# Performance work log

Hardware: AMD Instinct MI355X
Metric: run time of the kernel (lower is better)

The kernel has to match this reference:

```python
import jax, jax.numpy as jnp
import numpy as np


def setup_inputs() -> dict:
    key = jax.random.key(0)
    k1, k2, k3 = jax.random.split(key, 3)
    x = jax.random.normal(k1, (128, 3, 16, 64, 64), dtype=jnp.float32)
    conv_weight = jax.random.normal(k2, (24, 3, 3, 3, 3), dtype=jnp.float32) * 0.1
    conv_bias = jax.random.normal(k3, (24,), dtype=jnp.float32) * 0.1
    return {"x": x, "conv_weight": conv_weight, "conv_bias": conv_bias}


def reference(x, conv_weight, conv_bias):
    # Conv3d, stride=1, padding=0 (VALID), dilation=1, groups=1, NCDHW layout
    y = jax.lax.conv_general_dilated(
        x, conv_weight,
        window_strides=(1, 1, 1),
        padding='VALID',
        dimension_numbers=('NCDHW', 'OIDHW', 'NCDHW'),
    )
    y = y + conv_bias[None, :, None, None, None]  # [B, 24, 14, 62, 62]
    y = jnp.min(y, axis=2)                        # min over depth -> [B, 24, 62, 62]
    return jax.nn.softmax(y, axis=1)              # softmax over channels
```

## Files before the change

### kernel.cpp

```cpp
#include <hip/hip_runtime.h>
#include <math.h>

#define CIN   3
#define DIN   16
#define HWIN  64
#define COUT  24
#define DOUT  14
#define HOUT  62
#define WOUT  62

#define TILE_H  4
#define NTILES  16
#define NTHR    384
#define ROWS_IN 6
#define RP      68
#define PLANE_F (CIN * ROWS_IN * RP)
#define XSLAB_F (DIN * PLANE_F)
#define WOFF    XSLAB_F
#define WQ_F    324
#define LDS_F   (XSLAB_F + 6 * WQ_F)
#define SM_RP     64
#define SM_STRIDE (TILE_H * SM_RP)


__device__ __forceinline__ void gload_lds_dw(const float* g, float* l) {
    __builtin_amdgcn_global_load_lds(
        (const __attribute__((address_space(1))) unsigned int*)g,
        (__attribute__((address_space(3))) unsigned int*)l, 4, 0, 0);
}

__global__ __launch_bounds__(NTHR, 1) void conv_min_softmax_v6(
    const float* __restrict__ x,
    const float* __restrict__ w,
    const float* __restrict__ bias,
    float* __restrict__ out)
{
    __shared__ __align__(16) float smem[LDS_F];

    const int tid  = threadIdx.x;
    const int bid  = blockIdx.x;
    const int rt   = bid & (NTILES - 1);
    const int b    = bid >> 4;

    const int q    = __builtin_amdgcn_readfirstlane(tid >> 6);
    const int lane = tid & 63;
    const int r    = lane >> 4;
    const int wg   = lane & 15;
    const int q4   = q * 4;

    for (int i = tid; i < COUT * 81; i += NTHR) {
        const int co   = i / 81;
        const int rem  = i % 81;
        const int cin  = rem / 27;
        const int rem2 = rem % 27;
        const int kd   = rem2 / 9;
        const int kh   = (rem2 % 9) / 3;
        const int kw   = rem2 % 3;
        smem[WOFF + (co >> 2) * WQ_F + (cin * 3 + kh) * 36 + (kd * 3 + kw) * 4 + (co & 3)] = w[i];
    }
    const float bia0 = bias[q4 + 0], bia1 = bias[q4 + 1],
                bia2 = bias[q4 + 2], bia3 = bias[q4 + 3];

    const int grow = min(rt * TILE_H + q, HWIN - 1);
    const float* __restrict__ xrow =
        x + (size_t)b * (CIN * DIN * HWIN * HWIN) + grow * HWIN + lane;
    #pragma unroll
    for (int c = 0; c < CIN; ++c)
        #pragma unroll
        for (int p = 0; p < DIN; ++p)
            gload_lds_dw(xrow + (c * DIN + p) * (HWIN * HWIN),
                         &smem[p * PLANE_F + (c * ROWS_IN + q) * RP]);

    __syncthreads();

    float m[4][4];
    #pragma unroll
    for (int cop = 0; cop < 4; ++cop)
        #pragma unroll
        for (int i = 0; i < 4; ++i) m[cop][i] = 1e30f;

    const int vbase = r * RP + wg * 4;
    const float* __restrict__ wqb = &smem[WOFF + q * WQ_F];

    #pragma unroll 1
    for (int ch = 0; ch < 2; ++ch) {
        const int p0 = 7 * ch;

        float acc[7][4][4];
        #pragma unroll
        for (int d = 0; d < 7; ++d)
            #pragma unroll
            for (int cop = 0; cop < 4; ++cop)
                #pragma unroll
                for (int i = 0; i < 4; ++i) acc[d][cop][i] = 0.f;

        #pragma unroll 1
        for (int cin = 0; cin < CIN; ++cin) {
            #pragma unroll 1
            for (int kh = 0; kh < 3; ++kh) {
                const float* __restrict__ bp =
                    &smem[p0 * PLANE_F + cin * (ROWS_IN * RP) + kh * RP + vbase];
                const float* __restrict__ wp = wqb + (cin * 3 + kh) * 36;

                float wv[9][4];
                #pragma unroll
                for (int t = 0; t < 9; ++t)
                    *(float4*)wv[t] = *(const float4*)(wp + t * 4);

                #pragma unroll
                for (int pp = 0; pp < 9; ++pp) {
                    const float* rp2 = bp + pp * PLANE_F;
                    const float4 a4 = *(const float4*)rp2;
                    const float2 a2 = *(const float2*)(rp2 + 4);
                    const float xr[6] = { a4.x, a4.y, a4.z, a4.w, a2.x, a2.y };
                    #pragma unroll
                    for (int kd = 0; kd < 3; ++kd) {
                        if (pp - kd < 0 || pp - kd > 6) continue;
                        const int dzr = pp - kd;
                        #pragma unroll
                        for (int kw = 0; kw < 3; ++kw) {
                            #pragma unroll
                            for (int cop = 0; cop < 4; ++cop) {
                                const float wvv = wv[kd * 3 + kw][cop];
                                #pragma unroll
                                for (int i = 0; i < 4; ++i)
                                    acc[dzr][cop][i] = fmaf(wvv, xr[i + kw], acc[dzr][cop][i]);
                            }
                        }
                    }
                }
            }
        }

        #pragma unroll
        for (int d = 0; d < 7; ++d)
            #pragma unroll
            for (int cop = 0; cop < 4; ++cop)
                #pragma unroll
                for (int i = 0; i < 4; ++i)
                    m[cop][i] = fminf(m[cop][i], acc[d][cop][i]);
    }

    __syncthreads();

    {
        const int p = r * SM_RP + wg * 4;
        float4 v0 = { m[0][0] + bia0, m[0][1] + bia0, m[0][2] + bia0, m[0][3] + bia0 };
        float4 v1 = { m[1][0] + bia1, m[1][1] + bia1, m[1][2] + bia1, m[1][3] + bia1 };
        float4 v2 = { m[2][0] + bia2, m[2][1] + bia2, m[2][2] + bia2, m[2][3] + bia2 };
        float4 v3 = { m[3][0] + bia3, m[3][1] + bia3, m[3][2] + bia3, m[3][3] + bia3 };
        *(float4*)&smem[(q4 + 0) * SM_STRIDE + p] = v0;
        *(float4*)&smem[(q4 + 1) * SM_STRIDE + p] = v1;
        *(float4*)&smem[(q4 + 2) * SM_STRIDE + p] = v2;
        *(float4*)&smem[(q4 + 3) * SM_STRIDE + p] = v3;
    }
    __syncthreads();

    if (tid < 256) {
        const int row = tid >> 6;
        const int col = tid & 63;
        const int ho  = rt * TILE_H + row;
        if (col < WOUT && ho < HOUT) {
            float v[COUT];
            float mx = -1e30f;
            #pragma unroll
            for (int c = 0; c < COUT; ++c) {
                v[c] = smem[c * SM_STRIDE + row * SM_RP + col];
                mx = fmaxf(mx, v[c]);
            }
            float s = 0.f;
            #pragma unroll
            for (int c = 0; c < COUT; ++c) { v[c] = __expf(v[c] - mx); s += v[c]; }
            const float inv = 1.f / s;
            float* ob = out + (size_t)b * COUT * (HOUT * WOUT) + ho * WOUT + col;
            #pragma unroll
            for (int c = 0; c < COUT; ++c)
                ob[(size_t)c * (HOUT * WOUT)] = v[c] * inv;
        }
    }
}

extern "C" void kernel_launch(void* const* d_in, const int* in_sizes, int n_in,
                              void* d_out, int out_size, void* d_ws, size_t ws_size,
                              hipStream_t stream) {
    const float* x    = (const float*)d_in[0];
    const float* w    = (const float*)d_in[1];
    const float* bias = (const float*)d_in[2];
    float* out = (float*)d_out;

    conv_min_softmax_v6<<<128 * NTILES, NTHR, 0, stream>>>(x, w, bias, out);
}
```

Before: 498.3 us.

## Split output channels across eight waves, three per wave, with smaller depth chunks

Moves from 6 waves of 4 output channels each to 8 waves of 3 channels each (512 threads). The depth loop is split into chunks of 4,4,3,3 so the accumulator arrays shrink, and launch bounds request 2 blocks per CU. The input-slab load is redistributed across all 8 waves. The goal is more waves in flight per CU to hide LDS and FMA latency. The cost is that each weight float4 load now carries only 3 useful lanes, more halo input rows are reloaded across the smaller chunks, and LDS use per block may limit residency to one block.

Measured after the change: 476.8 us. 4.3% less time.

```diff
diff --git a/kernel.cpp b/kernel.cpp
--- a/kernel.cpp
+++ b/kernel.cpp
@@ -11,14 +11,14 @@
 
 #define TILE_H  4
 #define NTILES  16
-#define NTHR    384
+#define NTHR    512
 #define ROWS_IN 6
 #define RP      68
 #define PLANE_F (CIN * ROWS_IN * RP)
 #define XSLAB_F (DIN * PLANE_F)
 #define WOFF    XSLAB_F
-#define WQ_F    324
-#define LDS_F   (XSLAB_F + 6 * WQ_F)
+#define WT_F    324
+#define LDS_F   (XSLAB_F + 8 * WT_F)
 #define SM_RP     64
 #define SM_STRIDE (TILE_H * SM_RP)
 
@@ -29,7 +29,65 @@
         (__attribute__((address_space(3))) unsigned int*)l, 4, 0, 0);
 }
 
-__global__ __launch_bounds__(NTHR, 1) void conv_min_softmax_v6(
+template<int C>
+__device__ __forceinline__ void do_chunk(const float* __restrict__ xv,
+                                         const float* __restrict__ wqb,
+                                         float (&m)[3][4], const int p0)
+{
+    float acc[C][3][4];
+    #pragma unroll
+    for (int d = 0; d < C; ++d)
+        #pragma unroll
+        for (int cop = 0; cop < 3; ++cop)
+            #pragma unroll
+            for (int i = 0; i < 4; ++i) acc[d][cop][i] = 0.f;
+
+    #pragma unroll 1
+    for (int cin = 0; cin < CIN; ++cin) {
+        #pragma unroll 1
+        for (int kh = 0; kh < 3; ++kh) {
+            const float* __restrict__ bp = xv + p0 * PLANE_F + cin * (ROWS_IN * RP) + kh * RP;
+            const float* __restrict__ wp = wqb + (cin * 3 + kh) * 36;
+
+            float4 wv[9];
+            #pragma unroll
+            for (int t = 0; t < 9; ++t) wv[t] = *(const float4*)(wp + t * 4);
+
+            #pragma unroll
+            for (int pp = 0; pp < C + 2; ++pp) {
+                const float* rp2 = bp + pp * PLANE_F;
+                const float4 a4 = *(const float4*)rp2;
+                const float2 a2 = *(const float2*)(rp2 + 4);
+                const float xr[6] = { a4.x, a4.y, a4.z, a4.w, a2.x, a2.y };
+                #pragma unroll
+                for (int kd = 0; kd < 3; ++kd) {
+                    const int d = pp - kd;
+                    if (d < 0 || d >= C) continue;
+                    #pragma unroll
+                    for (int kw = 0; kw < 3; ++kw) {
+                        const float4 wt = wv[kd * 3 + kw];
+                        const float wc[3] = { wt.x, wt.y, wt.z };
+                        #pragma unroll
+                        for (int cop = 0; cop < 3; ++cop)
+                            #pragma unroll
+                            for (int i = 0; i < 4; ++i)
+                                acc[d][cop][i] = fmaf(wc[cop], xr[i + kw], acc[d][cop][i]);
+                    }
+                }
+            }
+        }
+    }
+
+    #pragma unroll
+    for (int d = 0; d < C; ++d)
+        #pragma unroll
+        for (int cop = 0; cop < 3; ++cop)
+            #pragma unroll
+            for (int i = 0; i < 4; ++i)
+                m[cop][i] = fminf(m[cop][i], acc[d][cop][i]);
+}
+
+__global__ __launch_bounds__(NTHR, 2) void conv_min_softmax_v7(
     const float* __restrict__ x,
     const float* __restrict__ w,
     const float* __restrict__ bias,
@@ -46,7 +104,7 @@
     const int lane = tid & 63;
     const int r    = lane >> 4;
     const int wg   = lane & 15;
-    const int q4   = q * 4;
+    const int q3   = q * 3;
 
     for (int i = tid; i < COUT * 81; i += NTHR) {
         const int co   = i / 81;
@@ -56,103 +114,50 @@
         const int kd   = rem2 / 9;
         const int kh   = (rem2 % 9) / 3;
         const int kw   = rem2 % 3;
-        smem[WOFF + (co >> 2) * WQ_F + (cin * 3 + kh) * 36 + (kd * 3 + kw) * 4 + (co & 3)] = w[i];
+        smem[WOFF + (co / 3) * WT_F + (cin * 3 + kh) * 36 + (kd * 3 + kw) * 4 + (co % 3)] = w[i];
     }
-    const float bia0 = bias[q4 + 0], bia1 = bias[q4 + 1],
-                bia2 = bias[q4 + 2], bia3 = bias[q4 + 3];
+    const float bia[3] = { bias[q3 + 0], bias[q3 + 1], bias[q3 + 2] };
 
-    const int grow = min(rt * TILE_H + q, HWIN - 1);
-    const float* __restrict__ xrow =
-        x + (size_t)b * (CIN * DIN * HWIN * HWIN) + grow * HWIN + lane;
-    #pragma unroll
-    for (int c = 0; c < CIN; ++c)
+    {
+        const float* __restrict__ xb =
+            x + (size_t)b * (CIN * DIN * HWIN * HWIN) + lane;
         #pragma unroll
-        for (int p = 0; p < DIN; ++p)
-            gload_lds_dw(xrow + (c * DIN + p) * (HWIN * HWIN),
-                         &smem[p * PLANE_F + (c * ROWS_IN + q) * RP]);
-
+        for (int k = 0; k < 36; ++k) {
+            const int p    = 2 * q + (k >= 18 ? 1 : 0);
+            const int sub  = k % 18;
+            const int cin  = sub / 6;
+            const int row  = sub % 6;
+            const int grow = min(rt * TILE_H + row, HWIN - 1);
+            gload_lds_dw(xb + ((cin * DIN + p) * (HWIN * HWIN) + grow * HWIN),
+                         &smem[p * PLANE_F + (cin * ROWS_IN + row) * RP]);
+        }
+    }
     __syncthreads();
 
-    float m[4][4];
+    float m[3][4];
     #pragma unroll
-    for (int cop = 0; cop < 4; ++cop)
+    for (int cop = 0; cop < 3; ++cop)
         #pragma unroll
         for (int i = 0; i < 4; ++i) m[cop][i] = 1e30f;
 
-    const int vbase = r * RP + wg * 4;
-    const float* __restrict__ wqb = &smem[WOFF + q * WQ_F];
+    const float* __restrict__ xv  = &smem[r * RP + wg * 4];
+    const float* __restrict__ wqb = &smem[WOFF + q * WT_F];
 
-    #pragma unroll 1
-    for (int ch = 0; ch < 2; ++ch) {
-        const int p0 = 7 * ch;
-
-        float acc[7][4][4];
-        #pragma unroll
-        for (int d = 0; d < 7; ++d)
-            #pragma unroll
-            for (int cop = 0; cop < 4; ++cop)
-                #pragma unroll
-                for (int i = 0; i < 4; ++i) acc[d][cop][i] = 0.f;
-
-        #pragma unroll 1
-        for (int cin = 0; cin < CIN; ++cin) {
-            #pragma unroll 1
-            for (int kh = 0; kh < 3; ++kh) {
-                const float* __restrict__ bp =
-                    &smem[p0 * PLANE_F + cin * (ROWS_IN * RP) + kh * RP + vbase];
-                const float* __restrict__ wp = wqb + (cin * 3 + kh) * 36;
-
-                float wv[9][4];
-                #pragma unroll
-                for (int t = 0; t < 9; ++t)
-                    *(float4*)wv[t] = *(const float4*)(wp + t * 4);
-
-                #pragma unroll
-                for (int pp = 0; pp < 9; ++pp) {
-                    const float* rp2 = bp + pp * PLANE_F;
-                    const float4 a4 = *(const float4*)rp2;
-                    const float2 a2 = *(const float2*)(rp2 + 4);
-                    const float xr[6] = { a4.x, a4.y, a4.z, a4.w, a2.x, a2.y };
-                    #pragma unroll
-                    for (int kd = 0; kd < 3; ++kd) {
-                        if (pp - kd < 0 || pp - kd > 6) continue;
-                        const int dzr = pp - kd;
-                        #pragma unroll
-                        for (int kw = 0; kw < 3; ++kw) {
-                            #pragma unroll
-                            for (int cop = 0; cop < 4; ++cop) {
-                                const float wvv = wv[kd * 3 + kw][cop];
-                                #pragma unroll
-                                for (int i = 0; i < 4; ++i)
-                                    acc[dzr][cop][i] = fmaf(wvv, xr[i + kw], acc[dzr][cop][i]);
-                            }
-                        }
-                    }
-                }
-            }
-        }
-
-        #pragma unroll
-        for (int d = 0; d < 7; ++d)
-            #pragma unroll
-            for (int cop = 0; cop < 4; ++cop)
-                #pragma unroll
-                for (int i = 0; i < 4; ++i)
-                    m[cop][i] = fminf(m[cop][i], acc[d][cop][i]);
-    }
+    do_chunk<4>(xv, wqb, m, 0);
+    do_chunk<4>(xv, wqb, m, 4);
+    do_chunk<3>(xv, wqb, m, 8);
+    do_chunk<3>(xv, wqb, m, 11);
 
     __syncthreads();
 
     {
         const int p = r * SM_RP + wg * 4;
-        float4 v0 = { m[0][0] + bia0, m[0][1] + bia0, m[0][2] + bia0, m[0][3] + bia0 };
-        float4 v1 = { m[1][0] + bia1, m[1][1] + bia1, m[1][2] + bia1, m[1][3] + bia1 };
-        float4 v2 = { m[2][0] + bia2, m[2][1] + bia2, m[2][2] + bia2, m[2][3] + bia2 };
-        float4 v3 = { m[3][0] + bia3, m[3][1] + bia3, m[3][2] + bia3, m[3][3] + bia3 };
-        *(float4*)&smem[(q4 + 0) * SM_STRIDE + p] = v0;
-        *(float4*)&smem[(q4 + 1) * SM_STRIDE + p] = v1;
-        *(float4*)&smem[(q4 + 2) * SM_STRIDE + p] = v2;
-        *(float4*)&smem[(q4 + 3) * SM_STRIDE + p] = v3;
+        #pragma unroll
+        for (int cop = 0; cop < 3; ++cop) {
+            float4 v = { m[cop][0] + bia[cop], m[cop][1] + bia[cop],
+                         m[cop][2] + bia[cop], m[cop][3] + bia[cop] };
+            *(float4*)&smem[(q3 + cop) * SM_STRIDE + p] = v;
+        }
     }
     __syncthreads();
 
@@ -188,5 +193,5 @@
     const float* bias = (const float*)d_in[2];
     float* out = (float*)d_out;
 
-    conv_min_softmax_v6<<<128 * NTILES, NTHR, 0, stream>>>(x, w, bias, out);
+    conv_min_softmax_v7<<<128 * NTILES, NTHR, 0, stream>>>(x, w, bias, out);
 }
```
